# Kernel tuning notes

Measured on AMD Instinct MI355X. Metric: run time of the kernel, lower is better.

Reference implementation:

```python
import jax, jax.numpy as jnp
import numpy as np

B, S, D, H = 2, 2048, 1024, 16
HD = D // H  # head_size = 64

def setup_inputs() -> dict:
    key = jax.random.key(0)
    ks = jax.random.split(key, 8)
    sc = 0.02
    return {
        "q": jax.random.normal(ks[0], (B, S, D), jnp.float32),
        "k": jax.random.normal(ks[1], (B, S, D), jnp.float32),
        "v": jax.random.normal(ks[2], (B, S, D), jnp.float32),
        "padding_mask": jnp.zeros((B, 1, 1, S), jnp.float32),
        "Wq": jax.random.normal(ks[3], (D, D), jnp.float32) * sc,
        "bq": jnp.zeros((D,), jnp.float32),
        "Wk": jax.random.normal(ks[4], (D, D), jnp.float32) * sc,
        "bk": jnp.zeros((D,), jnp.float32),
        "Wv": jax.random.normal(ks[5], (D, D), jnp.float32) * sc,
        "bv": jnp.zeros((D,), jnp.float32),
        "Wo": jax.random.normal(ks[6], (D, D), jnp.float32) * sc,
        "bo": jnp.zeros((D,), jnp.float32),
    }

def reference(q, k, v, padding_mask, Wq, bq, Wk, bk, Wv, bv, Wo, bo):
    b = q.shape[0]
    qh = (q @ Wq + bq).reshape(b, -1, H, HD)
    kh = (k @ Wk + bk).reshape(b, -1, H, HD)
    vh = (v @ Wv + bv).reshape(b, -1, H, HD)
    # [B, H, Sq, Sk] scores, materialized as in the original
    qk = jnp.einsum('bjhd,bkhd->bhjk', qh, kh) / jnp.sqrt(jnp.float32(HD))
    qk = qk + padding_mask * -1e12
    attn = jax.nn.softmax(qk, axis=-1)
    qkv = jnp.einsum('bhjk,bkhd->bjhd', attn, vh).reshape(b, -1, D)
    return qkv @ Wo + bo
```

## Files before the change

### kernel.cpp

```cpp
#include <hip/hip_runtime.h>
#include <math.h>

typedef __bf16 bf16_t;
typedef __bf16 bf16x8 __attribute__((ext_vector_type(8)));
typedef __bf16 bf16x4v __attribute__((ext_vector_type(4)));
typedef float f32x4 __attribute__((ext_vector_type(4)));

#define LOG2E 1.4426950408889634f

#if __has_builtin(__builtin_amdgcn_exp2f)
#define EXP2F(x) __builtin_amdgcn_exp2f(x)
#else
#define EXP2F(x) exp2f(x)
#endif

typedef __attribute__((address_space(1))) const unsigned int g_u32;
typedef __attribute__((address_space(3))) unsigned int l_u32;
__device__ __forceinline__ void load_lds_16B(const void* g, void* l){
  __builtin_amdgcn_global_load_lds((g_u32*)g, (l_u32*)l, 16, 0, 0);
}

__global__ __launch_bounds__(256) void cast3_kernel(const float* __restrict__ q,
                                                    const float* __restrict__ k,
                                                    const float* __restrict__ v,
                                                    bf16_t* __restrict__ out){
  int z = blockIdx.y;
  const float* x = (z == 0) ? q : (z == 1) ? k : v;
  int i = blockIdx.x * 256 + threadIdx.x;
  float4 f = reinterpret_cast<const float4*>(x)[i];
  bf16x4v w;
  w[0] = (bf16_t)f.x; w[1] = (bf16_t)f.y; w[2] = (bf16_t)f.z; w[3] = (bf16_t)f.w;
  reinterpret_cast<bf16x4v*>(out + (size_t)z * 4194304)[i] = w;
}

__global__ __launch_bounds__(256) void wtrans4_kernel(const float* __restrict__ Wq,
                                                      const float* __restrict__ Wk,
                                                      const float* __restrict__ Wv,
                                                      const float* __restrict__ Wo,
                                                      bf16_t* __restrict__ Wcat,
                                                      bf16_t* __restrict__ Wot){
  __shared__ float T[32][33];
  int z = blockIdx.z;
  const float* W = (z == 0) ? Wq : (z == 1) ? Wk : (z == 2) ? Wv : Wo;
  bf16_t* dst = (z < 3) ? (Wcat + (size_t)z * 1024 * 1024) : Wot;
  int x = threadIdx.x, y = threadIdx.y;
  int k0 = blockIdx.y * 32, n0 = blockIdx.x * 32;
  #pragma unroll
  for (int i = 0; i < 4; i++) T[y + 8*i][x] = W[(size_t)(k0 + y + 8*i) * 1024 + n0 + x];
  __syncthreads();
  #pragma unroll
  for (int i = 0; i < 4; i++) dst[(size_t)(n0 + y + 8*i) * 1024 + k0 + x] = (bf16_t)T[x][y + 8*i];
}

__global__ __launch_bounds__(256) void gemm_qkv_bf(const bf16_t* __restrict__ qkvin,
                                                   const bf16_t* __restrict__ Wcat,
                                                   const float* __restrict__ bq,
                                                   const float* __restrict__ bk,
                                                   const float* __restrict__ bv,
                                                   bf16_t* __restrict__ Cqkv){
  const int K = 1024, CS = 3072;
  __shared__ __align__(16) bf16_t As[128*32];
  __shared__ __align__(16) bf16_t Bs[128*32];
  int tid = threadIdx.x, wave = tid >> 6, lane = tid & 63;
  int l16 = lane & 15, lq = lane >> 4;
  int n0g = blockIdx.x * 128;
  int seg = n0g >> 10;
  const bf16_t* A   = qkvin + (size_t)seg * 4194304;
  const float* bias = (seg == 0) ? bq : (seg == 1) ? bk : bv;
  float scale = (seg == 0) ? 0.125f : 1.0f;
  int m0 = blockIdx.y * 128;
  int wm = (wave >> 1) * 64, wn = (wave & 1) * 64;
  int cposR = lq ^ ((l16 >> 2) & 3);
  f32x4 acc[4][4] = {};
  for (int kt = 0; kt < K; kt += 32){
    __syncthreads();
    #pragma unroll
    for (int i = 0; i < 2; i++){
      int u = tid + 256*i;
      int r = u >> 2, cpos = u & 3, cg = cpos ^ ((r >> 2) & 3);
      int ldsoff = (wave*64 + 256*i) * 16;
      load_lds_16B(&A[(size_t)(m0 + r) * K + kt + cg*8], (char*)As + ldsoff);
      load_lds_16B(&Wcat[(size_t)(n0g + r) * K + kt + cg*8], (char*)Bs + ldsoff);
    }
    __syncthreads();
    bf16x8 af[4], bfr[4];
    #pragma unroll
    for (int t = 0; t < 4; t++) af[t]  = *reinterpret_cast<bf16x8*>(&As[(wm + t*16 + l16)*32 + cposR*8]);
    #pragma unroll
    for (int t = 0; t < 4; t++) bfr[t] = *reinterpret_cast<bf16x8*>(&Bs[(wn + t*16 + l16)*32 + cposR*8]);
    #pragma unroll
    for (int ti = 0; ti < 4; ti++)
      #pragma unroll
      for (int tj = 0; tj < 4; tj++)
        acc[ti][tj] = __builtin_amdgcn_mfma_f32_16x16x32_bf16(af[ti], bfr[tj], acc[ti][tj], 0, 0, 0);
  }
  #pragma unroll
  for (int ti = 0; ti < 4; ti++){
    #pragma unroll
    for (int tj = 0; tj < 4; tj++){
      int col = n0g + wn + tj*16 + l16;
      float bvv = bias[col & 1023];
      #pragma unroll
      for (int r = 0; r < 4; r++){
        int row = m0 + wm + ti*16 + lq*4 + r;
        Cqkv[(size_t)row * CS + col] = (bf16_t)((acc[ti][tj][r] + bvv) * scale);
      }
    }
  }
}

__global__ __launch_bounds__(256) void gemm_qkv_f32(const float* __restrict__ qi,
                                                    const float* __restrict__ ki,
                                                    const float* __restrict__ vi,
                                                    const bf16_t* __restrict__ Wcat,
                                                    const float* __restrict__ bq,
                                                    const float* __restrict__ bk,
                                                    const float* __restrict__ bv,
                                                    bf16_t* __restrict__ Cqkv){
  const int K = 1024, CS = 3072;
  __shared__ __align__(16) float  Asf[128*32];
  __shared__ __align__(16) bf16_t Bs[128*32];
  int tid = threadIdx.x, wave = tid >> 6, lane = tid & 63;
  int l16 = lane & 15, lq = lane >> 4;
  int n0g = blockIdx.x * 128;
  int seg = n0g >> 10;
  const float* A    = (seg == 0) ? qi : (seg == 1) ? ki : vi;
  const float* bias = (seg == 0) ? bq : (seg == 1) ? bk : bv;
  float scale = (seg == 0) ? 0.125f : 1.0f;
  int m0 = blockIdx.y * 128;
  int wm = (wave >> 1) * 64, wn = (wave & 1) * 64;
  int cposR = lq ^ ((l16 >> 2) & 3);
  int ca0 = (2*lq)     ^ (l16 & 7);
  int ca1 = (2*lq + 1) ^ (l16 & 7);
  f32x4 acc[4][4] = {};
  for (int kt = 0; kt < K; kt += 32){
    __syncthreads();
    #pragma unroll
    for (int i = 0; i < 4; i++){
      int u = tid + 256*i;
      int r = u >> 3, cpos = u & 7, cg = cpos ^ (r & 7);
      load_lds_16B(&A[(size_t)(m0 + r) * K + kt + cg*4], (char*)Asf + (wave*64 + 256*i)*16);
    }
    #pragma unroll
    for (int i = 0; i < 2; i++){
      int u = tid + 256*i;
      int r = u >> 2, cpos = u & 3, cg = cpos ^ ((r >> 2) & 3);
      load_lds_16B(&Wcat[(size_t)(n0g + r) * K + kt + cg*8], (char*)Bs + (wave*64 + 256*i)*16);
    }
    __syncthreads();
    bf16x8 af[4], bfr[4];
    #pragma unroll
    for (int t = 0; t < 4; t++){
      int row = wm + t*16 + l16;
      f32x4 x0 = *reinterpret_cast<f32x4*>(&Asf[row*32 + ca0*4]);
      f32x4 x1 = *reinterpret_cast<f32x4*>(&Asf[row*32 + ca1*4]);
      bf16x8 a;
      a[0] = (bf16_t)x0[0]; a[1] = (bf16_t)x0[1]; a[2] = (bf16_t)x0[2]; a[3] = (bf16_t)x0[3];
      a[4] = (bf16_t)x1[0]; a[5] = (bf16_t)x1[1]; a[6] = (bf16_t)x1[2]; a[7] = (bf16_t)x1[3];
      af[t] = a;
    }
    #pragma unroll
    for (int t = 0; t < 4; t++) bfr[t] = *reinterpret_cast<bf16x8*>(&Bs[(wn + t*16 + l16)*32 + cposR*8]);
    #pragma unroll
    for (int ti = 0; ti < 4; ti++)
      #pragma unroll
      for (int tj = 0; tj < 4; tj++)
        acc[ti][tj] = __builtin_amdgcn_mfma_f32_16x16x32_bf16(af[ti], bfr[tj], acc[ti][tj], 0, 0, 0);
  }
  #pragma unroll
  for (int ti = 0; ti < 4; ti++){
    #pragma unroll
    for (int tj = 0; tj < 4; tj++){
      int col = n0g + wn + tj*16 + l16;
      float bvv = bias[col & 1023];
      #pragma unroll
      for (int r = 0; r < 4; r++){
        int row = m0 + wm + ti*16 + lq*4 + r;
        Cqkv[(size_t)row * CS + col] = (bf16_t)((acc[ti][tj][r] + bvv) * scale);
      }
    }
  }
}

__global__ __launch_bounds__(256) void gemm_out(const bf16_t* __restrict__ A,
                                                const bf16_t* __restrict__ Bt,
                                                const float* __restrict__ bias,
                                                float* __restrict__ C){
  const int K = 1024, N = 1024;
  __shared__ __align__(16) bf16_t As[128*64];
  __shared__ __align__(16) bf16_t Bs[64*64];
  int tid = threadIdx.x, wave = tid >> 6, lane = tid & 63;
  int l16 = lane & 15, lq = lane >> 4;
  int m0 = blockIdx.y * 128, n0 = blockIdx.x * 64;
  int wm = wave * 32;
  f32x4 acc[2][4] = {};
  for (int kt = 0; kt < K; kt += 64){
    __syncthreads();
    #pragma unroll
    for (int i = 0; i < 4; i++){
      int u = tid + 256*i;
      int r = u >> 3, cpos = u & 7, cg = cpos ^ (r & 7);
      load_lds_16B(&A[(size_t)(m0 + r) * K + kt + cg*8], (char*)As + (wave*64 + 256*i)*16);
    }
    #pragma unroll
    for (int i = 0; i < 2; i++){
      int u = tid + 256*i;
      int r = u >> 3, cpos = u & 7, cg = cpos ^ (r & 7);
      load_lds_16B(&Bt[(size_t)(n0 + r) * K + kt + cg*8], (char*)Bs + (wave*64 + 256*i)*16);
    }
    __syncthreads();
    #pragma unroll
    for (int kk = 0; kk < 2; kk++){
      bf16x8 af[2], bfr[4];
      #pragma unroll
      for (int t = 0; t < 2; t++){
        int row = wm + t*16 + l16, cpos = (kk*4 + lq) ^ (l16 & 7);
        af[t] = *reinterpret_cast<bf16x8*>(&As[row*64 + cpos*8]);
      }
      #pragma unroll
      for (int t = 0; t < 4; t++){
        int row = t*16 + l16, cpos = (kk*4 + lq) ^ (l16 & 7);
        bfr[t] = *reinterpret_cast<bf16x8*>(&Bs[row*64 + cpos*8]);
      }
      #pragma unroll
      for (int ti = 0; ti < 2; ti++)
        #pragma unroll
        for (int tj = 0; tj < 4; tj++)
          acc[ti][tj] = __builtin_amdgcn_mfma_f32_16x16x32_bf16(af[ti], bfr[tj], acc[ti][tj], 0, 0, 0);
    }
  }
  #pragma unroll
  for (int ti = 0; ti < 2; ti++){
    #pragma unroll
    for (int tj = 0; tj < 4; tj++){
      int col = n0 + tj*16 + l16;
      float bvv = bias[col];
      #pragma unroll
      for (int r = 0; r < 4; r++){
        int row = m0 + wm + ti*16 + lq*4 + r;
        C[(size_t)row * N + col] = acc[ti][tj][r] + bvv;
      }
    }
  }
}

__global__ __launch_bounds__(256) void vtrans_kernel(const bf16_t* __restrict__ qkv,
                                                     bf16_t* __restrict__ Vt){
  __shared__ bf16_t T[64][72];
  int tid = threadIdx.x;
  int s0 = blockIdx.x * 64, h = blockIdx.y, b = blockIdx.z;
  #pragma unroll
  for (int i = 0; i < 2; i++){
    int u = tid + 256*i;
    int r = u >> 3, c = (u & 7) * 8;
    *reinterpret_cast<uint4*>(&T[r][c]) =
      *reinterpret_cast<const uint4*>(&qkv[(size_t)(b*2048 + s0 + r) * 3072 + 2048 + h*64 + c]);
  }
  __syncthreads();
  #pragma unroll
  for (int i = 0; i < 2; i++){
    int u = tid + 256*i;
    int d = u >> 3, cs = (u & 7) * 8;
    bf16_t t8[8];
    #pragma unroll
    for (int j = 0; j < 8; j++) t8[j] = T[cs + j][d];
    *reinterpret_cast<uint4*>(&Vt[(size_t)((b*16 + h)*64 + d) * 2048 + s0 + cs]) =
      *reinterpret_cast<uint4*>(t8);
  }
}

__global__ __launch_bounds__(256) void attn_kernel(const bf16_t* __restrict__ qkv,
                                                   const bf16_t* __restrict__ vt,
                                                   const float* __restrict__ mask,
                                                   bf16_t* __restrict__ ctx){
  const int S = 2048, DS = 3072, D = 1024, HD = 64;
  __shared__ __align__(16) char smem[25600];
  bf16_t* Qs  = (bf16_t*)smem;
  bf16_t* Ps  = (bf16_t*)smem;
  bf16_t* Ks  = (bf16_t*)(smem + 9216);
  bf16_t* Vts = (bf16_t*)(smem + 17408);
  int tid = threadIdx.x, wave = tid >> 6, lane = tid & 63;
  int l16 = lane & 15, lq = lane >> 4;
  int qt = blockIdx.x, h = blockIdx.y, b = blockIdx.z;
  const bf16_t* Qg = qkv + (size_t)b*S*DS + h*HD;
  const bf16_t* Kg = qkv + (size_t)b*S*DS + 1024 + h*HD;
  const bf16_t* Vg = vt + (size_t)(b*16 + h)*HD*S;

  #pragma unroll
  for (int i = 0; i < 2; i++){
    int u = tid + 256*i;
    int r = u >> 3, cpos = u & 7, cg = cpos ^ (r & 7);
    load_lds_16B(&Qg[(size_t)(qt*64 + r) * DS + cg*8], smem + (wave*64 + 256*i)*16);
  }
  __syncthreads();
  bf16x8 qf[2];
  #pragma unroll
  for (int kk = 0; kk < 2; kk++){
    int row = wave*16 + l16;
    int cpos = (kk*4 + lq) ^ (l16 & 7);
    qf[kk] = *reinterpret_cast<bf16x8*>(&Qs[row*64 + cpos*8]);
  }
  f32x4 o[4] = {};
  f32x4 ol = {};
  bf16x8 ones;
  #pragma unroll
  for (int j = 0; j < 8; j++) ones[j] = (bf16_t)1.0f;

  for (int kt = 0; kt < S; kt += 64){
    __syncthreads();
    #pragma unroll
    for (int i = 0; i < 2; i++){
      int u = tid + 256*i;
      int r = u >> 3, cpos = u & 7, cg = cpos ^ (r & 7);
      load_lds_16B(&Kg[(size_t)(kt + r) * DS + cg*8], (char*)Ks + (wave*64 + 256*i)*16);
    }
    #pragma unroll
    for (int i = 0; i < 2; i++){
      int u = tid + 256*i;
      int r = u >> 3, cpos = u & 7, cg = cpos ^ (r & 7);
      load_lds_16B(&Vg[(size_t)r * S + kt + cg*8], (char*)Vts + (wave*64 + 256*i)*16);
    }
    __syncthreads();

    f32x4 sc[4];
    #pragma unroll
    for (int kk = 0; kk < 2; kk++){
      bf16x8 kf[4];
      #pragma unroll
      for (int tj = 0; tj < 4; tj++){
        int row = tj*16 + l16;
        int cpos = (kk*4 + lq) ^ (l16 & 7);
        kf[tj] = *reinterpret_cast<bf16x8*>(&Ks[row*64 + cpos*8]);
      }
      #pragma unroll
      for (int tj = 0; tj < 4; tj++){
        if (kk == 0){
          f32x4 z = {0.f, 0.f, 0.f, 0.f};
          sc[tj] = __builtin_amdgcn_mfma_f32_16x16x32_bf16(kf[tj], qf[0], z, 0, 0, 0);
        } else {
          sc[tj] = __builtin_amdgcn_mfma_f32_16x16x32_bf16(kf[tj], qf[1], sc[tj], 0, 0, 0);
        }
      }
    }
    int prow = wave*16 + l16;
    #pragma unroll
    for (int tj = 0; tj < 4; tj++){
      float4 mv = *reinterpret_cast<const float4*>(&mask[(size_t)b*S + kt + tj*16 + lq*4]);
      float p0 = EXP2F(fmaf(sc[tj][0], LOG2E, mv.x * (-1e12f * LOG2E)));
      float p1 = EXP2F(fmaf(sc[tj][1], LOG2E, mv.y * (-1e12f * LOG2E)));
      float p2 = EXP2F(fmaf(sc[tj][2], LOG2E, mv.z * (-1e12f * LOG2E)));
      float p3 = EXP2F(fmaf(sc[tj][3], LOG2E, mv.w * (-1e12f * LOG2E)));
      bf16x4v w;
      w[0] = (bf16_t)p0; w[1] = (bf16_t)p1; w[2] = (bf16_t)p2; w[3] = (bf16_t)p3;
      *reinterpret_cast<bf16x4v*>(&Ps[prow*72 + tj*16 + lq*4]) = w;
    }
    #pragma unroll
    for (int kk = 0; kk < 2; kk++){
      bf16x8 pf = *reinterpret_cast<bf16x8*>(&Ps[(wave*16 + l16)*72 + kk*32 + lq*8]);
      bf16x8 vf[4];
      #pragma unroll
      for (int dj = 0; dj < 4; dj++){
        int row = dj*16 + l16;
        int cpos = (kk*4 + lq) ^ (l16 & 7);
        vf[dj] = *reinterpret_cast<bf16x8*>(&Vts[row*64 + cpos*8]);
      }
      #pragma unroll
      for (int dj = 0; dj < 4; dj++)
        o[dj] = __builtin_amdgcn_mfma_f32_16x16x32_bf16(pf, vf[dj], o[dj], 0, 0, 0);
      ol = __builtin_amdgcn_mfma_f32_16x16x32_bf16(pf, ones, ol, 0, 0, 0);
    }
  }
  #pragma unroll
  for (int r = 0; r < 4; r++){
    float linv = 1.f / ol[r];
    int row = qt*64 + wave*16 + lq*4 + r;
    #pragma unroll
    for (int dj = 0; dj < 4; dj++)
      ctx[(size_t)(b*S + row) * D + h*HD + dj*16 + l16] = (bf16_t)(o[dj][r] * linv);
  }
}

extern "C" void kernel_launch(void* const* d_in, const int* in_sizes, int n_in,
                              void* d_out, int out_size, void* d_ws, size_t ws_size,
                              hipStream_t stream){
  const float* q    = (const float*)d_in[0];
  const float* k    = (const float*)d_in[1];
  const float* v    = (const float*)d_in[2];
  const float* mask = (const float*)d_in[3];
  const float* Wq   = (const float*)d_in[4];
  const float* bq   = (const float*)d_in[5];
  const float* Wk   = (const float*)d_in[6];
  const float* bk   = (const float*)d_in[7];
  const float* Wv   = (const float*)d_in[8];
  const float* bv   = (const float*)d_in[9];
  const float* Wo   = (const float*)d_in[10];
  const float* bo   = (const float*)d_in[11];

  char* ws = (char*)d_ws;
  bf16_t* qkv   = (bf16_t*)(ws);
  bf16_t* Wcat  = (bf16_t*)(ws + 25165824);
  bf16_t* Wot   = (bf16_t*)(ws + 31457280);
  bf16_t* Vt    = (bf16_t*)(ws + 33554432);
  bf16_t* ctx   = (bf16_t*)(ws + 41943040);
  bf16_t* qkvin = (bf16_t*)(ws + 33554432);

  wtrans4_kernel<<<dim3(32,32,4), dim3(32,8), 0, stream>>>(Wq, Wk, Wv, Wo, Wcat, Wot);
  if (ws_size >= 58720256){
    cast3_kernel<<<dim3(4096,3), 256, 0, stream>>>(q, k, v, qkvin);
    gemm_qkv_bf<<<dim3(24,32), 256, 0, stream>>>(qkvin, Wcat, bq, bk, bv, qkv);
  } else {
    gemm_qkv_f32<<<dim3(24,32), 256, 0, stream>>>(q, k, v, Wcat, bq, bk, bv, qkv);
  }
  vtrans_kernel<<<dim3(32,16,2), 256, 0, stream>>>(qkv, Vt);
  attn_kernel<<<dim3(32,16,2), 256, 0, stream>>>(qkv, Vt, mask, ctx);
  gemm_out<<<dim3(16,32), 256, 0, stream>>>(ctx, Wot, bo, (float*)d_out);
}
```

Baseline: 241.9 us.

## Fuse V transpose into QKV GEMM epilogue and restructure attention with 32x32 MFMA split-K

The QKV projection now writes Q, K into separate contiguous buffers and writes V directly in transposed per-head layout, removing the separate vtrans kernel. The attention kernel switches to 32x32x16 MFMA tiles, splits each 64-key tile across two wave pairs, computes row sums with scalar adds instead of an extra ones-MFMA, and reduces partial outputs through LDS at the end. Q is prescaled by log2e so exp2 needs no extra multiply. Risks include scattered 2-byte stores in the V epilogue and the added LDS reduction pass.

After: 268.7 us. +11.1%, slower.

```diff
diff --git a/kernel.cpp b/kernel.cpp
--- a/kernel.cpp
+++ b/kernel.cpp
@@ -5,8 +5,10 @@
 typedef __bf16 bf16x8 __attribute__((ext_vector_type(8)));
 typedef __bf16 bf16x4v __attribute__((ext_vector_type(4)));
 typedef float f32x4 __attribute__((ext_vector_type(4)));
+typedef float f32x16 __attribute__((ext_vector_type(16)));
 
 #define LOG2E 1.4426950408889634f
+#define MBIAS_C (-1e12f * LOG2E)
 
 #if __has_builtin(__builtin_amdgcn_exp2f)
 #define EXP2F(x) __builtin_amdgcn_exp2f(x)
@@ -18,6 +20,13 @@
 typedef __attribute__((address_space(3))) unsigned int l_u32;
 __device__ __forceinline__ void load_lds_16B(const void* g, void* l){
   __builtin_amdgcn_global_load_lds((g_u32*)g, (l_u32*)l, 16, 0, 0);
+}
+
+__device__ __forceinline__ f32x16 zero16(){
+  f32x16 z;
+  #pragma unroll
+  for (int i = 0; i < 16; i++) z[i] = 0.f;
+  return z;
 }
 
 __global__ __launch_bounds__(256) void cast3_kernel(const float* __restrict__ q,
@@ -52,13 +61,54 @@
   for (int i = 0; i < 4; i++) dst[(size_t)(n0 + y + 8*i) * 1024 + k0 + x] = (bf16_t)T[x][y + 8*i];
 }
 
+__device__ __forceinline__ void qkv_epilogue(f32x4 (&acc)[4][4], int seg, int n0g, int m0,
+                                             int wm, int wn, int l16, int lq,
+                                             const float* bias, bf16_t* qp, bf16_t* kp,
+                                             bf16_t* Vt){
+  if (seg < 2){
+    bf16_t* Cp = (seg == 0) ? qp : kp;
+    float scale = (seg == 0) ? 0.125f * LOG2E : 1.0f;
+    #pragma unroll
+    for (int ti = 0; ti < 4; ti++){
+      #pragma unroll
+      for (int tj = 0; tj < 4; tj++){
+        int col = (n0g + wn + tj*16 + l16) & 1023;
+        float bvv = bias[col];
+        #pragma unroll
+        for (int r = 0; r < 4; r++){
+          int row = m0 + wm + ti*16 + lq*4 + r;
+          Cp[(size_t)row * 1024 + col] = (bf16_t)((acc[ti][tj][r] + bvv) * scale);
+        }
+      }
+    }
+  } else {
+    #pragma unroll
+    for (int ti = 0; ti < 4; ti++){
+      #pragma unroll
+      for (int tj = 0; tj < 4; tj++){
+        int dg = (n0g - 2048) + wn + tj*16 + l16;
+        int h = dg >> 6, dl = dg & 63;
+        float bvv = bias[dg];
+        #pragma unroll
+        for (int r = 0; r < 4; r++){
+          int row = m0 + wm + ti*16 + lq*4 + r;
+          int b = row >> 11, s = row & 2047;
+          Vt[(size_t)((b*16 + h)*64 + dl) * 2048 + s] = (bf16_t)(acc[ti][tj][r] + bvv);
+        }
+      }
+    }
+  }
+}
+
 __global__ __launch_bounds__(256) void gemm_qkv_bf(const bf16_t* __restrict__ qkvin,
                                                    const bf16_t* __restrict__ Wcat,
                                                    const float* __restrict__ bq,
                                                    const float* __restrict__ bk,
                                                    const float* __restrict__ bv,
-                                                   bf16_t* __restrict__ Cqkv){
-  const int K = 1024, CS = 3072;
+                                                   bf16_t* __restrict__ qp,
+                                                   bf16_t* __restrict__ kp,
+                                                   bf16_t* __restrict__ Vt){
+  const int K = 1024;
   __shared__ __align__(16) bf16_t As[128*32];
   __shared__ __align__(16) bf16_t Bs[128*32];
   int tid = threadIdx.x, wave = tid >> 6, lane = tid & 63;
@@ -67,7 +117,6 @@
   int seg = n0g >> 10;
   const bf16_t* A   = qkvin + (size_t)seg * 4194304;
   const float* bias = (seg == 0) ? bq : (seg == 1) ? bk : bv;
-  float scale = (seg == 0) ? 0.125f : 1.0f;
   int m0 = blockIdx.y * 128;
   int wm = (wave >> 1) * 64, wn = (wave & 1) * 64;
   int cposR = lq ^ ((l16 >> 2) & 3);
@@ -94,19 +143,7 @@
       for (int tj = 0; tj < 4; tj++)
         acc[ti][tj] = __builtin_amdgcn_mfma_f32_16x16x32_bf16(af[ti], bfr[tj], acc[ti][tj], 0, 0, 0);
   }
-  #pragma unroll
-  for (int ti = 0; ti < 4; ti++){
-    #pragma unroll
-    for (int tj = 0; tj < 4; tj++){
-      int col = n0g + wn + tj*16 + l16;
-      float bvv = bias[col & 1023];
-      #pragma unroll
-      for (int r = 0; r < 4; r++){
-        int row = m0 + wm + ti*16 + lq*4 + r;
-        Cqkv[(size_t)row * CS + col] = (bf16_t)((acc[ti][tj][r] + bvv) * scale);
-      }
-    }
-  }
+  qkv_epilogue(acc, seg, n0g, m0, wm, wn, l16, lq, bias, qp, kp, Vt);
 }
 
 __global__ __launch_bounds__(256) void gemm_qkv_f32(const float* __restrict__ qi,
@@ -116,8 +153,10 @@
                                                     const float* __restrict__ bq,
                                                     const float* __restrict__ bk,
                                                     const float* __restrict__ bv,
-                                                    bf16_t* __restrict__ Cqkv){
-  const int K = 1024, CS = 3072;
+                                                    bf16_t* __restrict__ qp,
+                                                    bf16_t* __restrict__ kp,
+                                                    bf16_t* __restrict__ Vt){
+  const int K = 1024;
   __shared__ __align__(16) float  Asf[128*32];
   __shared__ __align__(16) bf16_t Bs[128*32];
   int tid = threadIdx.x, wave = tid >> 6, lane = tid & 63;
@@ -126,7 +165,6 @@
   int seg = n0g >> 10;
   const float* A    = (seg == 0) ? qi : (seg == 1) ? ki : vi;
   const float* bias = (seg == 0) ? bq : (seg == 1) ? bk : bv;
-  float scale = (seg == 0) ? 0.125f : 1.0f;
   int m0 = blockIdx.y * 128;
   int wm = (wave >> 1) * 64, wn = (wave & 1) * 64;
   int cposR = lq ^ ((l16 >> 2) & 3);
@@ -167,19 +205,7 @@
       for (int tj = 0; tj < 4; tj++)
         acc[ti][tj] = __builtin_amdgcn_mfma_f32_16x16x32_bf16(af[ti], bfr[tj], acc[ti][tj], 0, 0, 0);
   }
-  #pragma unroll
-  for (int ti = 0; ti < 4; ti++){
-    #pragma unroll
-    for (int tj = 0; tj < 4; tj++){
-      int col = n0g + wn + tj*16 + l16;
-      float bvv = bias[col & 1023];
-      #pragma unroll
-      for (int r = 0; r < 4; r++){
-        int row = m0 + wm + ti*16 + lq*4 + r;
-        Cqkv[(size_t)row * CS + col] = (bf16_t)((acc[ti][tj][r] + bvv) * scale);
-      }
-    }
-  }
+  qkv_epilogue(acc, seg, n0g, m0, wm, wn, l16, lq, bias, qp, kp, Vt);
 }
 
 __global__ __launch_bounds__(256) void gemm_out(const bf16_t* __restrict__ A,
@@ -244,139 +270,127 @@
   }
 }
 
-__global__ __launch_bounds__(256) void vtrans_kernel(const bf16_t* __restrict__ qkv,
-                                                     bf16_t* __restrict__ Vt){
-  __shared__ bf16_t T[64][72];
-  int tid = threadIdx.x;
-  int s0 = blockIdx.x * 64, h = blockIdx.y, b = blockIdx.z;
-  #pragma unroll
-  for (int i = 0; i < 2; i++){
-    int u = tid + 256*i;
-    int r = u >> 3, c = (u & 7) * 8;
-    *reinterpret_cast<uint4*>(&T[r][c]) =
-      *reinterpret_cast<const uint4*>(&qkv[(size_t)(b*2048 + s0 + r) * 3072 + 2048 + h*64 + c]);
-  }
-  __syncthreads();
-  #pragma unroll
-  for (int i = 0; i < 2; i++){
-    int u = tid + 256*i;
-    int d = u >> 3, cs = (u & 7) * 8;
-    bf16_t t8[8];
-    #pragma unroll
-    for (int j = 0; j < 8; j++) t8[j] = T[cs + j][d];
-    *reinterpret_cast<uint4*>(&Vt[(size_t)((b*16 + h)*64 + d) * 2048 + s0 + cs]) =
-      *reinterpret_cast<uint4*>(t8);
-  }
-}
-
-__global__ __launch_bounds__(256) void attn_kernel(const bf16_t* __restrict__ qkv,
+__global__ __launch_bounds__(256) void attn_kernel(const bf16_t* __restrict__ qp,
+                                                   const bf16_t* __restrict__ kp,
                                                    const bf16_t* __restrict__ vt,
                                                    const float* __restrict__ mask,
                                                    bf16_t* __restrict__ ctx){
-  const int S = 2048, DS = 3072, D = 1024, HD = 64;
-  __shared__ __align__(16) char smem[25600];
-  bf16_t* Qs  = (bf16_t*)smem;
-  bf16_t* Ps  = (bf16_t*)smem;
-  bf16_t* Ks  = (bf16_t*)(smem + 9216);
-  bf16_t* Vts = (bf16_t*)(smem + 17408);
+  const int S = 2048, D = 1024, HD = 64;
+  __shared__ __align__(16) char smem[26624];
+  bf16_t* Qs   = (bf16_t*)smem;
+  bf16_t* Ps   = (bf16_t*)smem;
+  bf16_t* Ks   = (bf16_t*)(smem + 10240);
+  bf16_t* Vts  = (bf16_t*)(smem + 18432);
+  float* Opart = (float*)smem;
+  float* Lsum  = (float*)(smem + 16384);
+  float* Lcomb = (float*)(smem + 16640);
   int tid = threadIdx.x, wave = tid >> 6, lane = tid & 63;
-  int l16 = lane & 15, lq = lane >> 4;
+  int l32 = lane & 31, H = lane >> 5;
+  int qhalf = wave & 1, khalf = wave >> 1;
   int qt = blockIdx.x, h = blockIdx.y, b = blockIdx.z;
-  const bf16_t* Qg = qkv + (size_t)b*S*DS + h*HD;
-  const bf16_t* Kg = qkv + (size_t)b*S*DS + 1024 + h*HD;
+  const bf16_t* Qg = qp + (size_t)b*S*D + h*HD;
+  const bf16_t* Kg = kp + (size_t)b*S*D + h*HD;
   const bf16_t* Vg = vt + (size_t)(b*16 + h)*HD*S;
 
   #pragma unroll
   for (int i = 0; i < 2; i++){
     int u = tid + 256*i;
-    int r = u >> 3, cpos = u & 7, cg = cpos ^ (r & 7);
-    load_lds_16B(&Qg[(size_t)(qt*64 + r) * DS + cg*8], smem + (wave*64 + 256*i)*16);
+    int r = u >> 3, c = u & 7, cg = c ^ (r & 7);
+    load_lds_16B(&Qg[(size_t)(qt*64 + r) * D + cg*8], smem + (wave*64 + 256*i)*16);
   }
   __syncthreads();
-  bf16x8 qf[2];
-  #pragma unroll
-  for (int kk = 0; kk < 2; kk++){
-    int row = wave*16 + l16;
-    int cpos = (kk*4 + lq) ^ (l16 & 7);
-    qf[kk] = *reinterpret_cast<bf16x8*>(&Qs[row*64 + cpos*8]);
-  }
-  f32x4 o[4] = {};
-  f32x4 ol = {};
-  bf16x8 ones;
-  #pragma unroll
-  for (int j = 0; j < 8; j++) ones[j] = (bf16_t)1.0f;
+  int qrow = qhalf*32 + l32;
+  bf16x8 qf[4];
+  #pragma unroll
+  for (int s = 0; s < 4; s++){
+    int c = 2*s + H;
+    qf[s] = *reinterpret_cast<bf16x8*>(&Qs[qrow*64 + (c ^ (qrow & 7))*8]);
+  }
+  f32x16 o0 = zero16(), o1 = zero16();
+  float lacc = 0.f;
+  int krow = khalf*32 + l32;
+  bf16_t* Pw = Ps + wave*32*40;
 
   for (int kt = 0; kt < S; kt += 64){
     __syncthreads();
     #pragma unroll
     for (int i = 0; i < 2; i++){
       int u = tid + 256*i;
-      int r = u >> 3, cpos = u & 7, cg = cpos ^ (r & 7);
-      load_lds_16B(&Kg[(size_t)(kt + r) * DS + cg*8], (char*)Ks + (wave*64 + 256*i)*16);
+      int r = u >> 3, c = u & 7, cg = c ^ (r & 7);
+      load_lds_16B(&Kg[(size_t)(kt + r) * D + cg*8], (char*)Ks + (wave*64 + 256*i)*16);
     }
     #pragma unroll
     for (int i = 0; i < 2; i++){
       int u = tid + 256*i;
-      int r = u >> 3, cpos = u & 7, cg = cpos ^ (r & 7);
+      int r = u >> 3, c = u & 7, cg = c ^ (r & 7);
       load_lds_16B(&Vg[(size_t)r * S + kt + cg*8], (char*)Vts + (wave*64 + 256*i)*16);
     }
     __syncthreads();
 
-    f32x4 sc[4];
-    #pragma unroll
-    for (int kk = 0; kk < 2; kk++){
-      bf16x8 kf[4];
-      #pragma unroll
-      for (int tj = 0; tj < 4; tj++){
-        int row = tj*16 + l16;
-        int cpos = (kk*4 + lq) ^ (l16 & 7);
-        kf[tj] = *reinterpret_cast<bf16x8*>(&Ks[row*64 + cpos*8]);
-      }
-      #pragma unroll
-      for (int tj = 0; tj < 4; tj++){
-        if (kk == 0){
-          f32x4 z = {0.f, 0.f, 0.f, 0.f};
-          sc[tj] = __builtin_amdgcn_mfma_f32_16x16x32_bf16(kf[tj], qf[0], z, 0, 0, 0);
-        } else {
-          sc[tj] = __builtin_amdgcn_mfma_f32_16x16x32_bf16(kf[tj], qf[1], sc[tj], 0, 0, 0);
-        }
-      }
-    }
-    int prow = wave*16 + l16;
-    #pragma unroll
-    for (int tj = 0; tj < 4; tj++){
-      float4 mv = *reinterpret_cast<const float4*>(&mask[(size_t)b*S + kt + tj*16 + lq*4]);
-      float p0 = EXP2F(fmaf(sc[tj][0], LOG2E, mv.x * (-1e12f * LOG2E)));
-      float p1 = EXP2F(fmaf(sc[tj][1], LOG2E, mv.y * (-1e12f * LOG2E)));
-      float p2 = EXP2F(fmaf(sc[tj][2], LOG2E, mv.z * (-1e12f * LOG2E)));
-      float p3 = EXP2F(fmaf(sc[tj][3], LOG2E, mv.w * (-1e12f * LOG2E)));
+    f32x16 sc;
+    #pragma unroll
+    for (int s = 0; s < 4; s++){
+      int c = 2*s + H;
+      bf16x8 kf = *reinterpret_cast<bf16x8*>(&Ks[krow*64 + (c ^ (krow & 7))*8]);
+      if (s == 0) sc = __builtin_amdgcn_mfma_f32_32x32x16_bf16(kf, qf[0], zero16(), 0, 0, 0);
+      else        sc = __builtin_amdgcn_mfma_f32_32x32x16_bf16(kf, qf[s], sc, 0, 0, 0);
+    }
+    float lt = 0.f;
+    #pragma unroll
+    for (int g = 0; g < 4; g++){
+      int kcol = kt + khalf*32 + 8*g + 4*H;
+      float4 mv = *reinterpret_cast<const float4*>(&mask[(size_t)b*S + kcol]);
+      float p0 = EXP2F(fmaf(mv.x, MBIAS_C, sc[4*g+0]));
+      float p1 = EXP2F(fmaf(mv.y, MBIAS_C, sc[4*g+1]));
+      float p2 = EXP2F(fmaf(mv.z, MBIAS_C, sc[4*g+2]));
+      float p3 = EXP2F(fmaf(mv.w, MBIAS_C, sc[4*g+3]));
+      lt += (p0 + p1) + (p2 + p3);
       bf16x4v w;
       w[0] = (bf16_t)p0; w[1] = (bf16_t)p1; w[2] = (bf16_t)p2; w[3] = (bf16_t)p3;
-      *reinterpret_cast<bf16x4v*>(&Ps[prow*72 + tj*16 + lq*4]) = w;
-    }
-    #pragma unroll
-    for (int kk = 0; kk < 2; kk++){
-      bf16x8 pf = *reinterpret_cast<bf16x8*>(&Ps[(wave*16 + l16)*72 + kk*32 + lq*8]);
-      bf16x8 vf[4];
-      #pragma unroll
-      for (int dj = 0; dj < 4; dj++){
-        int row = dj*16 + l16;
-        int cpos = (kk*4 + lq) ^ (l16 & 7);
-        vf[dj] = *reinterpret_cast<bf16x8*>(&Vts[row*64 + cpos*8]);
-      }
-      #pragma unroll
-      for (int dj = 0; dj < 4; dj++)
-        o[dj] = __builtin_amdgcn_mfma_f32_16x16x32_bf16(pf, vf[dj], o[dj], 0, 0, 0);
-      ol = __builtin_amdgcn_mfma_f32_16x16x32_bf16(pf, ones, ol, 0, 0, 0);
-    }
-  }
-  #pragma unroll
-  for (int r = 0; r < 4; r++){
-    float linv = 1.f / ol[r];
-    int row = qt*64 + wave*16 + lq*4 + r;
-    #pragma unroll
-    for (int dj = 0; dj < 4; dj++)
-      ctx[(size_t)(b*S + row) * D + h*HD + dj*16 + l16] = (bf16_t)(o[dj][r] * linv);
+      *reinterpret_cast<bf16x4v*>(&Pw[l32*40 + 8*g + 4*H]) = w;
+    }
+    lt += __shfl_xor(lt, 32);
+    lacc += lt;
+    #pragma unroll
+    for (int ks = 0; ks < 2; ks++){
+      bf16x8 pf = *reinterpret_cast<bf16x8*>(&Pw[l32*40 + ks*16 + 8*H]);
+      int c0 = 4*khalf + 2*ks + H;
+      bf16x8 vf0 = *reinterpret_cast<bf16x8*>(&Vts[l32*64 + (c0 ^ (l32 & 7))*8]);
+      bf16x8 vf1 = *reinterpret_cast<bf16x8*>(&Vts[(32 + l32)*64 + (c0 ^ (l32 & 7))*8]);
+      o0 = __builtin_amdgcn_mfma_f32_32x32x16_bf16(pf, vf0, o0, 0, 0, 0);
+      o1 = __builtin_amdgcn_mfma_f32_32x32x16_bf16(pf, vf1, o1, 0, 0, 0);
+    }
+  }
+  __syncthreads();
+  if (khalf == 1){
+    #pragma unroll
+    for (int reg = 0; reg < 16; reg++){
+      Opart[qhalf*2048 + reg*64 + lane]        = o0[reg];
+      Opart[qhalf*2048 + 1024 + reg*64 + lane] = o1[reg];
+    }
+    Lsum[qhalf*32 + l32] = lacc;
+  }
+  __syncthreads();
+  if (khalf == 0){
+    #pragma unroll
+    for (int reg = 0; reg < 16; reg++){
+      o0[reg] += Opart[qhalf*2048 + reg*64 + lane];
+      o1[reg] += Opart[qhalf*2048 + 1024 + reg*64 + lane];
+    }
+    lacc += Lsum[qhalf*32 + l32];
+    Lcomb[qhalf*32 + l32] = lacc;
+    #pragma unroll
+    for (int g = 0; g < 4; g++){
+      f32x4 lv = *reinterpret_cast<f32x4*>(&Lcomb[qhalf*32 + 8*g + 4*H]);
+      #pragma unroll
+      for (int j = 0; j < 4; j++){
+        float inv = 1.f / lv[j];
+        int grow = qt*64 + qhalf*32 + 8*g + 4*H + j;
+        size_t base = (size_t)(b*S + grow) * D + h*HD;
+        ctx[base + l32]      = (bf16_t)(o0[4*g + j] * inv);
+        ctx[base + 32 + l32] = (bf16_t)(o1[4*g + j] * inv);
+      }
+    }
   }
 }
 
@@ -397,21 +411,21 @@
   const float* bo   = (const float*)d_in[11];
 
   char* ws = (char*)d_ws;
-  bf16_t* qkv   = (bf16_t*)(ws);
+  bf16_t* qp    = (bf16_t*)(ws);
+  bf16_t* kp    = (bf16_t*)(ws + 8388608);
+  bf16_t* Vt    = (bf16_t*)(ws + 16777216);
   bf16_t* Wcat  = (bf16_t*)(ws + 25165824);
   bf16_t* Wot   = (bf16_t*)(ws + 31457280);
-  bf16_t* Vt    = (bf16_t*)(ws + 33554432);
-  bf16_t* ctx   = (bf16_t*)(ws + 41943040);
+  bf16_t* ctx   = (bf16_t*)(ws + 33554432);
   bf16_t* qkvin = (bf16_t*)(ws + 33554432);
 
   wtrans4_kernel<<<dim3(32,32,4), dim3(32,8), 0, stream>>>(Wq, Wk, Wv, Wo, Wcat, Wot);
   if (ws_size >= 58720256){
     cast3_kernel<<<dim3(4096,3), 256, 0, stream>>>(q, k, v, qkvin);
-    gemm_qkv_bf<<<dim3(24,32), 256, 0, stream>>>(qkvin, Wcat, bq, bk, bv, qkv);
+    gemm_qkv_bf<<<dim3(24,32), 256, 0, stream>>>(qkvin, Wcat, bq, bk, bv, qp, kp, Vt);
   } else {
-    gemm_qkv_f32<<<dim3(24,32), 256, 0, stream>>>(q, k, v, Wcat, bq, bk, bv, qkv);
-  }
-  vtrans_kernel<<<dim3(32,16,2), 256, 0, stream>>>(qkv, Vt);
-  attn_kernel<<<dim3(32,16,2), 256, 0, stream>>>(qkv, Vt, mask, ctx);
+    gemm_qkv_f32<<<dim3(24,32), 256, 0, stream>>>(q, k, v, Wcat, bq, bk, bv, qp, kp, Vt);
+  }
+  attn_kernel<<<dim3(32,16,2), 256, 0, stream>>>(qp, kp, Vt, mask, ctx);
   gemm_out<<<dim3(16,32), 256, 0, stream>>>(ctx, Wot, bo, (float*)d_out);
 }
```
